# Kernel optimization log

Hardware: AMD Instinct MI355X
Metric: run time of the kernel (lower is better)

Reference implementation:

```python
import jax, jax.numpy as jnp
import numpy as np

N_NODES = 50000
N_EDGES = 800000
F_IN = 128      # n_alleles
HID = 64        # ge_hidden_dim
HEADS = 2       # gat_heads
LAT = 128       # latent_dim
N_PHEN = 50


def setup_inputs() -> dict:
    key = jax.random.key(0)
    ks = jax.random.split(key, 16)
    s = 0.05
    return {
        'x': jax.random.normal(ks[0], (N_NODES, F_IN), jnp.float32),
        'edge_index': jax.random.randint(ks[1], (2, N_EDGES), 0, N_NODES, jnp.int64),
        'pheno_idx': jnp.arange(N_PHEN, dtype=jnp.int64),
        'pheno_embedding': jax.random.normal(ks[2], (N_PHEN, F_IN), jnp.float32) * 0.1,
        'Wl1': jax.random.normal(ks[3], (F_IN, HEADS * HID), jnp.float32) * s,
        'Wr1': jax.random.normal(ks[4], (F_IN, HEADS * HID), jnp.float32) * s,
        'att1': jax.random.normal(ks[5], (HEADS, HID), jnp.float32) * s,
        'b1': jax.random.normal(ks[6], (HEADS * HID,), jnp.float32) * s,
        'Wl2': jax.random.normal(ks[7], (HEADS * HID, LAT), jnp.float32) * s,
        'Wr2': jax.random.normal(ks[8], (HEADS * HID, LAT), jnp.float32) * s,
        'att2': jax.random.normal(ks[9], (1, LAT), jnp.float32) * s,
        'b2': jax.random.normal(ks[10], (LAT,), jnp.float32) * s,
        'Wp': jax.random.normal(ks[11], (LAT, LAT), jnp.float32) * s,
        'bp': jax.random.normal(ks[12], (LAT,), jnp.float32) * s,
    }


def gatv2_conv(x, src, dst, Wl, Wr, att, bias, concat):
    # PyG GATv2Conv: e = att . leaky_relu(Wl x_src + Wr x_dst, 0.2), softmax over dst
    N = x.shape[0]
    H, C = att.shape
    xl = (x @ Wl).reshape(N, H, C)
    xr = (x @ Wr).reshape(N, H, C)
    feat = jax.nn.leaky_relu(xl[src] + xr[dst], 0.2)         # [E,H,C]
    logits = jnp.einsum('ehc,hc->eh', feat, att)             # [E,H]
    m = jax.ops.segment_max(logits, dst, num_segments=N)     # [N,H]
    ex = jnp.exp(logits - m[dst])
    denom = jax.ops.segment_sum(ex, dst, num_segments=N)
    alpha = ex / denom[dst]                                  # [E,H]
    out = jax.ops.segment_sum(alpha[:, :, None] * xl[src], dst, num_segments=N)
    out = out.reshape(N, H * C) if concat else out.mean(axis=1)
    return out + bias


def reference(x, edge_index, pheno_idx, pheno_embedding,
              Wl1, Wr1, att1, b1, Wl2, Wr2, att2, b2, Wp, bp):
    N = x.shape[0]
    # learnable phenotype node embeddings replace their input features
    x = x.at[pheno_idx].set(pheno_embedding)
    # PyG default: add self loops
    loops = jnp.arange(N, dtype=edge_index.dtype)
    src = jnp.concatenate([edge_index[0], loops])
    dst = jnp.concatenate([edge_index[1], loops])
    h = jax.nn.leaky_relu(gatv2_conv(x, src, dst, Wl1, Wr1, att1, b1, True), 0.01)
    h = gatv2_conv(h, src, dst, Wl2, Wr2, att2, b2, False)
    graph_embedding = h[pheno_idx].mean(axis=0, keepdims=True)  # [1, LAT]
    return graph_embedding @ Wp + bp
```

## Files before the change

### kernel.cpp

```cpp
#include <hip/hip_runtime.h>
#include <hip/hip_fp16.h>
#include <cstdint>

#define F_DIM 128

typedef _Float16 f16x8 __attribute__((ext_vector_type(8)));
typedef float f32x4 __attribute__((ext_vector_type(4)));

__device__ __forceinline__ float lrelu(float x, float s) { return x > 0.f ? x : s * x; }

template<int W>
__device__ __forceinline__ float redg(float p) {
  #pragma unroll
  for (int d = 1; d < W; d <<= 1) p += __shfl_xor(p, d);
  return p;
}

__device__ __forceinline__ int cidx(const int* __restrict__ csr, int k, int last) {
  return csr[k <= last ? k : last];
}

__device__ __forceinline__ __half2 shfl_xor_h2(__half2 v, int m) {
  union { __half2 h; int i; } u; u.h = v;
  u.i = __shfl_xor(u.i, m);
  return u.h;
}

typedef _Float16 h2v __attribute__((ext_vector_type(2)));
__device__ __forceinline__ __half2 h2max(__half2 a, __half2 b) {
  union { __half2 h; h2v v; } ua, ub, ur;
  ua.h = a; ub.h = b;
  ur.v = __builtin_elementwise_max(ua.v, ub.v);
  return ur.h;
}

__global__ void k_init(int* __restrict__ deg, int* __restrict__ rowmap, int N) {
  int i = blockIdx.x * blockDim.x + threadIdx.x;
  if (i < N) { deg[i] = 0; rowmap[i] = -1; }
}

__global__ void k_hist_rowmap(const int* __restrict__ dst, int* __restrict__ deg,
                              const int* __restrict__ pidx, int* __restrict__ rowmap,
                              int E, int P) {
  int e = blockIdx.x * blockDim.x + threadIdx.x;
  if (e < E) atomicAdd(&deg[dst[e]], 1);
  if (e < P) rowmap[pidx[e]] = e;
}

__global__ void k_scan_reduce(const int* __restrict__ deg, int* __restrict__ bsum, int N) {
  __shared__ int ts[256];
  int tid = threadIdx.x;
  int base = blockIdx.x * 1024 + tid * 4;
  int s = 0;
  #pragma unroll
  for (int j = 0; j < 4; ++j) { int idx = base + j; if (idx < N) s += deg[idx]; }
  ts[tid] = s; __syncthreads();
  for (int d = 128; d > 0; d >>= 1) { if (tid < d) ts[tid] += ts[tid + d]; __syncthreads(); }
  if (tid == 0) bsum[blockIdx.x] = ts[0];
}

__global__ void k_scan_single(int* __restrict__ bsum, int nb) {
  int l = threadIdx.x;
  int v = (l < nb) ? bsum[l] : 0;
  int orig = v;
  #pragma unroll
  for (int d = 1; d < 64; d <<= 1) { int t = __shfl_up(v, d); if (l >= d) v += t; }
  if (l < nb) bsum[l] = v - orig;
}

__global__ void k_scan_final(const int* __restrict__ deg, const int* __restrict__ bsum,
                             int* __restrict__ rowStart, int* __restrict__ cursor,
                             int N, int E) {
  __shared__ int ts[256];
  int tid = threadIdx.x;
  int base = blockIdx.x * 1024 + tid * 4;
  int v[4]; int s = 0;
  #pragma unroll
  for (int j = 0; j < 4; ++j) { int idx = base + j; v[j] = (idx < N) ? deg[idx] : 0; s += v[j]; }
  ts[tid] = s; __syncthreads();
  for (int d = 1; d < 256; d <<= 1) {
    int t = (tid >= d) ? ts[tid - d] : 0;
    __syncthreads();
    ts[tid] += t;
    __syncthreads();
  }
  int off = bsum[blockIdx.x] + ts[tid] - s;
  #pragma unroll
  for (int j = 0; j < 4; ++j) {
    int idx = base + j;
    if (idx < N) { rowStart[idx] = off; cursor[idx] = off; }
    off += v[j];
  }
  if (blockIdx.x == 0 && tid == 0) rowStart[N] = E;
}

__global__ void k_scatter_edges(const int* __restrict__ src, const int* __restrict__ dst,
                                int* __restrict__ cur, int* __restrict__ csr, int E) {
  int e = blockIdx.x * blockDim.x + threadIdx.x;
  if (e >= E) return;
  int d = dst[e];
  int p = atomicAdd(&cur[d], 1);
  csr[p] = src[e];
}

__global__ void k_cvt_x(const float* __restrict__ x, const float* __restrict__ pe,
                        const int* __restrict__ rowmap, __half* __restrict__ xh, int N) {
  int t = blockIdx.x * 256 + threadIdx.x;
  if (t >= N * 16) return;
  int row = t >> 4, seg = (t & 15) * 8;
  const float* src = &x[(size_t)row * 128 + seg];
  int rm = rowmap[row];
  if (rm >= 0) src = &pe[(size_t)rm * 128 + seg];
  float4 v0 = *reinterpret_cast<const float4*>(src);
  float4 v1 = *reinterpret_cast<const float4*>(src + 4);
  union { __half h[8]; float4 f; } pk;
  pk.h[0] = __float2half(v0.x); pk.h[1] = __float2half(v0.y);
  pk.h[2] = __float2half(v0.z); pk.h[3] = __float2half(v0.w);
  pk.h[4] = __float2half(v1.x); pk.h[5] = __float2half(v1.y);
  pk.h[6] = __float2half(v1.z); pk.h[7] = __float2half(v1.w);
  *reinterpret_cast<float4*>(&xh[(size_t)row * 128 + seg]) = pk.f;
}

__global__ void k_cvt_w(const float* __restrict__ Wl1, const float* __restrict__ Wr1,
                        const float* __restrict__ Wl2, const float* __restrict__ Wr2,
                        __half* __restrict__ Wt1, __half* __restrict__ Wt2) {
  int t = blockIdx.x * 256 + threadIdx.x;
  if (t >= 2 * 32768) return;
  int layer = t >> 15;
  int i = t & 32767;
  int c = i >> 7, k = i & 127;
  const float* Wl = layer ? Wl2 : Wl1;
  const float* Wr = layer ? Wr2 : Wr1;
  float v = (c < 128) ? Wl[k * 128 + c] : Wr[k * 128 + (c - 128)];
  (layer ? Wt2 : Wt1)[i] = __float2half(v);
}

__global__ __launch_bounds__(256) void k_gemm_mfma(
    const __half* __restrict__ Ah, const __half* __restrict__ Wt,
    __half* __restrict__ outL, __half* __restrict__ outR, int M)
{
  int cg = blockIdx.x & 3;
  int rg = blockIdx.x >> 2;
  int wv = threadIdx.x >> 6;
  int l  = threadIdx.x & 63;
  int rowb = rg * 128 + wv * 32;
  int colb = cg * 64;
  int lr = l & 15;
  int lq = l >> 4;
  f32x4 acc[2][4] = {};
  #pragma unroll
  for (int ks = 0; ks < 4; ++ks) {
    int k0 = ks * 32 + lq * 8;
    int r0 = rowb + lr;      if (r0 > M - 1) r0 = M - 1;
    int r1 = rowb + 16 + lr; if (r1 > M - 1) r1 = M - 1;
    f16x8 a0 = *reinterpret_cast<const f16x8*>(&Ah[(size_t)r0 * 128 + k0]);
    f16x8 a1 = *reinterpret_cast<const f16x8*>(&Ah[(size_t)r1 * 128 + k0]);
    f16x8 b[4];
    #pragma unroll
    for (int c = 0; c < 4; ++c)
      b[c] = *reinterpret_cast<const f16x8*>(&Wt[(size_t)(colb + c * 16 + lr) * 128 + k0]);
    #pragma unroll
    for (int c = 0; c < 4; ++c) {
      acc[0][c] = __builtin_amdgcn_mfma_f32_16x16x32_f16(a0, b[c], acc[0][c], 0, 0, 0);
      acc[1][c] = __builtin_amdgcn_mfma_f32_16x16x32_f16(a1, b[c], acc[1][c], 0, 0, 0);
    }
  }
  #pragma unroll
  for (int r = 0; r < 2; ++r) {
    #pragma unroll
    for (int j = 0; j < 4; ++j) {
      int grow = rowb + r * 16 + lq * 4 + j;
      if (grow < M) {
        #pragma unroll
        for (int c = 0; c < 4; ++c) {
          int gcol = colb + c * 16 + lr;
          __half v = __float2half(acc[r][c][j]);
          if (gcol < 128) outL[(size_t)grow * 128 + gcol] = v;
          else            outR[(size_t)grow * 128 + (gcol - 128)] = v;
        }
      }
    }
  }
}

template<int RW, bool OUTER_LRELU, bool HOUT>
__global__ __launch_bounds__(64) void k_agg(
    const __half* __restrict__ xl, const __half* __restrict__ xr,
    const float* __restrict__ att, const float* __restrict__ bias,
    const int* __restrict__ rowStart, const int* __restrict__ csr,
    float* __restrict__ outf, __half* __restrict__ outh, int N)
{
  int n = blockIdx.x;
  int l = threadIdx.x;
  int slot = l >> 4;
  int q = l & 15;
  int ch = q * 8;
  size_t nb = (size_t)n * F_DIM + ch;

  float4 rawr = *reinterpret_cast<const float4*>(&xr[nb]);
  float4 rawl = *reinterpret_cast<const float4*>(&xl[nb]);
  const __half2* xrn = reinterpret_cast<const __half2*>(&rawr);
  const __half2* xln = reinterpret_cast<const __half2*>(&rawl);
  __half2 av[4];
  #pragma unroll
  for (int i = 0; i < 4; ++i)
    av[i] = __float22half2_rn(*reinterpret_cast<const float2*>(&att[ch + 2 * i]));
  const __half2 slope = __float2half2_rn(0.2f);

  float denom;
  __half2 acc[4];
  {
    __half2 pr = __float2half2_rn(0.f);
    #pragma unroll
    for (int i = 0; i < 4; ++i) {
      __half2 t = __hadd2(xln[i], xrn[i]);
      __half2 lr = h2max(t, __hmul2(t, slope));
      pr = __hfma2(lr, av[i], pr);
    }
    float2 pf = __half22float2(pr);
    float p = redg<RW>(pf.x + pf.y);
    float w = (slot == 0) ? __expf(p) : 0.f;
    denom = w;
    __half2 wh = __float2half2_rn(w);
    #pragma unroll
    for (int i = 0; i < 4; ++i) acc[i] = __hmul2(xln[i], wh);
  }

  int e0 = rowStart[n], e1 = rowStart[n + 1];
  int last = e1 - 1;
  if (e0 < e1) {
    auto ld = [&](int k) {
      int s = cidx(csr, k, last);
      return *reinterpret_cast<const float4*>(&xl[(size_t)s * F_DIM + ch]);
    };
    auto proc = [&](float4 rawv, int ebase) {
      const __half2* xv = reinterpret_cast<const __half2*>(&rawv);
      __half2 pr = __float2half2_rn(0.f);
      #pragma unroll
      for (int i = 0; i < 4; ++i) {
        __half2 t = __hadd2(xv[i], xrn[i]);
        __half2 lr = h2max(t, __hmul2(t, slope));
        pr = __hfma2(lr, av[i], pr);
      }
      float2 pf = __half22float2(pr);
      float p = redg<RW>(pf.x + pf.y);
      float wE = ((ebase + slot) <= last) ? __expf(p) : 0.f;
      denom += wE;
      __half2 wh = __float2half2_rn(wE);
      #pragma unroll
      for (int i = 0; i < 4; ++i) acc[i] = __hfma2(xv[i], wh, acc[i]);
    };
    float4 v0 = ld(e0 + slot);
    float4 v1 = ld(e0 + 4 + slot);
    for (int e = e0; e < e1; e += 4) {
      bool m2 = (e + 8) < e1;
      float4 v2;
      if (m2) v2 = ld(e + 8 + slot);
      proc(v0, e);
      v0 = v1;
      if (m2) v1 = v2;
    }
  }

  denom += __shfl_xor(denom, 16);
  denom += __shfl_xor(denom, 32);
  #pragma unroll
  for (int i = 0; i < 4; ++i) {
    acc[i] = __hadd2(acc[i], shfl_xor_h2(acc[i], 16));
    acc[i] = __hadd2(acc[i], shfl_xor_h2(acc[i], 32));
  }

  if (slot == 0) {
    float inv = 1.0f / denom;
    float o[8];
    #pragma unroll
    for (int i = 0; i < 4; ++i) {
      float2 a2 = __half22float2(acc[i]);
      o[2 * i + 0] = fmaf(a2.x, inv, bias[ch + 2 * i + 0]);
      o[2 * i + 1] = fmaf(a2.y, inv, bias[ch + 2 * i + 1]);
    }
    if (OUTER_LRELU) {
      #pragma unroll
      for (int i = 0; i < 8; ++i) o[i] = lrelu(o[i], 0.01f);
    }
    if (HOUT) {
      union { __half h[8]; float4 f; } pk;
      #pragma unroll
      for (int i = 0; i < 8; ++i) pk.h[i] = __float2half(o[i]);
      *reinterpret_cast<float4*>(&outh[nb]) = pk.f;
    } else {
      *reinterpret_cast<float4*>(&outf[nb]) = *reinterpret_cast<float4*>(&o[0]);
      *reinterpret_cast<float4*>(&outf[nb + 4]) = *reinterpret_cast<float4*>(&o[4]);
    }
  }
}

__global__ void k_final(const float* __restrict__ h2, const int* __restrict__ pidx,
                        const float* __restrict__ Wp, const float* __restrict__ bp,
                        float* __restrict__ out, int P)
{
  __shared__ float ge[F_DIM];
  int t = threadIdx.x;
  float s0 = 0.f, s1 = 0.f;
  for (int i = 0; i + 1 < P; i += 2) {
    s0 += h2[(size_t)pidx[i] * F_DIM + t];
    s1 += h2[(size_t)pidx[i + 1] * F_DIM + t];
  }
  if (P & 1) s0 += h2[(size_t)pidx[P - 1] * F_DIM + t];
  ge[t] = (s0 + s1) / (float)P;
  __syncthreads();
  float a0 = 0.f, a1 = 0.f, a2 = 0.f, a3 = 0.f;
  for (int k = 0; k < F_DIM; k += 4) {
    a0 = fmaf(ge[k + 0], Wp[(k + 0) * F_DIM + t], a0);
    a1 = fmaf(ge[k + 1], Wp[(k + 1) * F_DIM + t], a1);
    a2 = fmaf(ge[k + 2], Wp[(k + 2) * F_DIM + t], a2);
    a3 = fmaf(ge[k + 3], Wp[(k + 3) * F_DIM + t], a3);
  }
  out[t] = bp[t] + ((a0 + a1) + (a2 + a3));
}

extern "C" void kernel_launch(void* const* d_in, const int* in_sizes, int n_in,
                              void* d_out, int out_size, void* d_ws, size_t ws_size,
                              hipStream_t stream)
{
  const float* x    = (const float*)d_in[0];
  const int*   ei   = (const int*)d_in[1];
  const int*   pidx = (const int*)d_in[2];
  const float* pe   = (const float*)d_in[3];
  const float* Wl1  = (const float*)d_in[4];
  const float* Wr1  = (const float*)d_in[5];
  const float* att1 = (const float*)d_in[6];
  const float* b1   = (const float*)d_in[7];
  const float* Wl2  = (const float*)d_in[8];
  const float* Wr2  = (const float*)d_in[9];
  const float* att2 = (const float*)d_in[10];
  const float* b2   = (const float*)d_in[11];
  const float* Wp   = (const float*)d_in[12];
  const float* bp   = (const float*)d_in[13];
  float* outp = (float*)d_out;

  const int N = in_sizes[0] / F_DIM;
  const int E = in_sizes[1] / 2;
  const int P = in_sizes[2];
  const int* esrc = ei;
  const int* edst = ei + E;

  char* w = (char*)d_ws;
  size_t off = 0;
  auto alloc = [&](size_t bytes) -> void* {
    void* p = w + off;
    off += (bytes + 255) & ~(size_t)255;
    return p;
  };
  const size_t NF = (size_t)N * F_DIM * sizeof(float);
  float*  A   = (float*)alloc(NF);
  __half* Bh  = (__half*)alloc(NF / 2);
  __half* Ch  = (__half*)alloc(NF / 2);
  __half* Xh  = (__half*)alloc(NF / 2);
  __half* H1h = (__half*)alloc(NF / 2);
  __half* Wt1 = (__half*)alloc(2 * 32768 * sizeof(__half));
  __half* Wt2 = Wt1 + 32768;
  int* rowStart = (int*)alloc((size_t)(N + 1) * sizeof(int));
  int* cursor   = (int*)alloc((size_t)N * sizeof(int));
  int* deg      = (int*)alloc((size_t)N * sizeof(int));
  int* bsum     = (int*)alloc(64 * sizeof(int));
  int* rowmap   = (int*)alloc((size_t)N * sizeof(int));
  int* csr      = (int*)alloc((size_t)E * sizeof(int));

  const int nb = (N + 1023) / 1024;
  const int RG = (N + 127) / 128;

  k_init<<<(N + 255) / 256, 256, 0, stream>>>(deg, rowmap, N);
  k_hist_rowmap<<<(E + 255) / 256, 256, 0, stream>>>(edst, deg, pidx, rowmap, E, P);
  k_scan_reduce<<<nb, 256, 0, stream>>>(deg, bsum, N);
  k_scan_single<<<1, 64, 0, stream>>>(bsum, nb);
  k_scan_final<<<nb, 256, 0, stream>>>(deg, bsum, rowStart, cursor, N, E);
  k_scatter_edges<<<(E + 255) / 256, 256, 0, stream>>>(esrc, edst, cursor, csr, E);

  k_cvt_x<<<(N * 16 + 255) / 256, 256, 0, stream>>>(x, pe, rowmap, Xh, N);
  k_cvt_w<<<256, 256, 0, stream>>>(Wl1, Wr1, Wl2, Wr2, Wt1, Wt2);

  k_gemm_mfma<<<RG * 4, 256, 0, stream>>>(Xh, Wt1, Bh, Ch, N);
  k_agg<8, true, true><<<N, 64, 0, stream>>>(Bh, Ch, att1, b1, rowStart, csr,
                                             nullptr, H1h, N);
  k_gemm_mfma<<<RG * 4, 256, 0, stream>>>(H1h, Wt2, Bh, Ch, N);
  k_agg<16, false, false><<<N, 64, 0, stream>>>(Bh, Ch, att2, b2, rowStart, csr,
                                                A, nullptr, N);
  k_final<<<1, 128, 0, stream>>>(A, pidx, Wp, bp, outp, P);
}
```

Baseline: 327.0 us.

## Partition edge histogram/scatter by XCD slot and fuse init/convert kernels

The histogram and edge-scatter kernels now assign blocks to eight destination-range slots (blockIdx mod 8), so that atomics on a given destination range come from blocks that likely run on the same XCD, which is meant to keep atomic traffic local to one L2. Every slot's blocks re-read the whole dst array, which multiplies index reads by eight. The init kernel is fused with the weight conversion, and the edge scatter is fused with the x conversion as separate block ranges, which cuts kernel launches and lets independent work overlap.

```diff
diff --git a/kernel.cpp b/kernel.cpp
--- a/kernel.cpp
+++ b/kernel.cpp
@@ -3,6 +3,7 @@
 #include <cstdint>
 
 #define F_DIM 128
+#define NSLOT 8
 
 typedef _Float16 f16x8 __attribute__((ext_vector_type(8)));
 typedef float f32x4 __attribute__((ext_vector_type(4)));
@@ -34,17 +35,41 @@
   return ur.h;
 }
 
-__global__ void k_init(int* __restrict__ deg, int* __restrict__ rowmap, int N) {
-  int i = blockIdx.x * blockDim.x + threadIdx.x;
-  if (i < N) { deg[i] = 0; rowmap[i] = -1; }
-}
-
-__global__ void k_hist_rowmap(const int* __restrict__ dst, int* __restrict__ deg,
-                              const int* __restrict__ pidx, int* __restrict__ rowmap,
-                              int E, int P) {
-  int e = blockIdx.x * blockDim.x + threadIdx.x;
-  if (e < E) atomicAdd(&deg[dst[e]], 1);
-  if (e < P) rowmap[pidx[e]] = e;
+__global__ void k_init_cvtw(int* __restrict__ deg, int* __restrict__ rowmap, int N, int NB1,
+                            const float* __restrict__ Wl1, const float* __restrict__ Wr1,
+                            const float* __restrict__ Wl2, const float* __restrict__ Wr2,
+                            __half* __restrict__ Wt1, __half* __restrict__ Wt2) {
+  int bid = blockIdx.x;
+  if (bid < NB1) {
+    int i = bid * 256 + threadIdx.x;
+    if (i < N) { deg[i] = 0; rowmap[i] = -1; }
+  } else {
+    int t = (bid - NB1) * 256 + threadIdx.x;
+    if (t < 2 * 32768) {
+      int layer = t >> 15;
+      int i = t & 32767;
+      int c = i >> 7, k = i & 127;
+      const float* Wl = layer ? Wl2 : Wl1;
+      const float* Wr = layer ? Wr2 : Wr1;
+      float v = (c < 128) ? Wl[k * 128 + c] : Wr[k * 128 + (c - 128)];
+      (layer ? Wt2 : Wt1)[i] = __float2half(v);
+    }
+  }
+}
+
+__global__ void k_hist_xcd(const int* __restrict__ dst, int* __restrict__ deg,
+                           const int* __restrict__ pidx, int* __restrict__ rowmap,
+                           int E, int P, int C, int span) {
+  if (blockIdx.x == 0) {
+    for (int i = threadIdx.x; i < P; i += 256) rowmap[pidx[i]] = i;
+  }
+  int s = blockIdx.x & (NSLOT - 1);
+  int cb = blockIdx.x >> 3;
+  int lo = s * span, hi = lo + span;
+  for (int e = cb * 256 + threadIdx.x; e < E; e += C * 256) {
+    int d = dst[e];
+    if (d >= lo && d < hi) atomicAdd(&deg[d], 1);
+  }
 }
 
 __global__ void k_scan_reduce(const int* __restrict__ deg, int* __restrict__ bsum, int N) {
@@ -94,45 +119,41 @@
   if (blockIdx.x == 0 && tid == 0) rowStart[N] = E;
 }
 
-__global__ void k_scatter_edges(const int* __restrict__ src, const int* __restrict__ dst,
-                                int* __restrict__ cur, int* __restrict__ csr, int E) {
-  int e = blockIdx.x * blockDim.x + threadIdx.x;
-  if (e >= E) return;
-  int d = dst[e];
-  int p = atomicAdd(&cur[d], 1);
-  csr[p] = src[e];
-}
-
-__global__ void k_cvt_x(const float* __restrict__ x, const float* __restrict__ pe,
-                        const int* __restrict__ rowmap, __half* __restrict__ xh, int N) {
-  int t = blockIdx.x * 256 + threadIdx.x;
-  if (t >= N * 16) return;
-  int row = t >> 4, seg = (t & 15) * 8;
-  const float* src = &x[(size_t)row * 128 + seg];
-  int rm = rowmap[row];
-  if (rm >= 0) src = &pe[(size_t)rm * 128 + seg];
-  float4 v0 = *reinterpret_cast<const float4*>(src);
-  float4 v1 = *reinterpret_cast<const float4*>(src + 4);
-  union { __half h[8]; float4 f; } pk;
-  pk.h[0] = __float2half(v0.x); pk.h[1] = __float2half(v0.y);
-  pk.h[2] = __float2half(v0.z); pk.h[3] = __float2half(v0.w);
-  pk.h[4] = __float2half(v1.x); pk.h[5] = __float2half(v1.y);
-  pk.h[6] = __float2half(v1.z); pk.h[7] = __float2half(v1.w);
-  *reinterpret_cast<float4*>(&xh[(size_t)row * 128 + seg]) = pk.f;
-}
-
-__global__ void k_cvt_w(const float* __restrict__ Wl1, const float* __restrict__ Wr1,
-                        const float* __restrict__ Wl2, const float* __restrict__ Wr2,
-                        __half* __restrict__ Wt1, __half* __restrict__ Wt2) {
-  int t = blockIdx.x * 256 + threadIdx.x;
-  if (t >= 2 * 32768) return;
-  int layer = t >> 15;
-  int i = t & 32767;
-  int c = i >> 7, k = i & 127;
-  const float* Wl = layer ? Wl2 : Wl1;
-  const float* Wr = layer ? Wr2 : Wr1;
-  float v = (c < 128) ? Wl[k * 128 + c] : Wr[k * 128 + (c - 128)];
-  (layer ? Wt2 : Wt1)[i] = __float2half(v);
+__global__ void k_scatter_xcd_cvtx(const int* __restrict__ src, const int* __restrict__ dst,
+                                   int* __restrict__ cur, int* __restrict__ csr,
+                                   int E, int C, int span, int N, int CVTB,
+                                   const float* __restrict__ x, const float* __restrict__ pe,
+                                   const int* __restrict__ rowmap, __half* __restrict__ xh) {
+  int bid = blockIdx.x;
+  int SC = NSLOT * C;
+  if (bid < SC) {
+    int s = bid & (NSLOT - 1);
+    int cb = bid >> 3;
+    int lo = s * span, hi = lo + span;
+    for (int e = cb * 256 + threadIdx.x; e < E; e += C * 256) {
+      int d = dst[e];
+      if (d >= lo && d < hi) {
+        int p = atomicAdd(&cur[d], 1);
+        csr[p] = src[e];
+      }
+    }
+  } else {
+    int nt = N * 16;
+    for (int t = (bid - SC) * 256 + threadIdx.x; t < nt; t += CVTB * 256) {
+      int row = t >> 4, seg = (t & 15) * 8;
+      const float* sp = &x[(size_t)row * 128 + seg];
+      int rm = rowmap[row];
+      if (rm >= 0) sp = &pe[(size_t)rm * 128 + seg];
+      float4 v0 = *reinterpret_cast<const float4*>(sp);
+      float4 v1 = *reinterpret_cast<const float4*>(sp + 4);
+      union { __half h[8]; float4 f; } pk;
+      pk.h[0] = __float2half(v0.x); pk.h[1] = __float2half(v0.y);
+      pk.h[2] = __float2half(v0.z); pk.h[3] = __float2half(v0.w);
+      pk.h[4] = __float2half(v1.x); pk.h[5] = __float2half(v1.y);
+      pk.h[6] = __float2half(v1.z); pk.h[7] = __float2half(v1.w);
+      *reinterpret_cast<float4*>(&xh[(size_t)row * 128 + seg]) = pk.f;
+    }
+  }
 }
 
 __global__ __launch_bounds__(256) void k_gemm_mfma(
@@ -367,18 +388,20 @@
   int* rowmap   = (int*)alloc((size_t)N * sizeof(int));
   int* csr      = (int*)alloc((size_t)E * sizeof(int));
 
-  const int nb = (N + 1023) / 1024;
-  const int RG = (N + 127) / 128;
-
-  k_init<<<(N + 255) / 256, 256, 0, stream>>>(deg, rowmap, N);
-  k_hist_rowmap<<<(E + 255) / 256, 256, 0, stream>>>(edst, deg, pidx, rowmap, E, P);
+  const int nb   = (N + 1023) / 1024;
+  const int RG   = (N + 127) / 128;
+  const int NB1  = (N + 255) / 256;
+  const int span = (N + NSLOT - 1) / NSLOT;
+  const int C    = 128;
+  const int CVTB = 1024;
+
+  k_init_cvtw<<<NB1 + 256, 256, 0, stream>>>(deg, rowmap, N, NB1, Wl1, Wr1, Wl2, Wr2, Wt1, Wt2);
+  k_hist_xcd<<<NSLOT * C, 256, 0, stream>>>(edst, deg, pidx, rowmap, E, P, C, span);
   k_scan_reduce<<<nb, 256, 0, stream>>>(deg, bsum, N);
   k_scan_single<<<1, 64, 0, stream>>>(bsum, nb);
   k_scan_final<<<nb, 256, 0, stream>>>(deg, bsum, rowStart, cursor, N, E);
-  k_scatter_edges<<<(E + 255) / 256, 256, 0, stream>>>(esrc, edst, cursor, csr, E);
-
-  k_cvt_x<<<(N * 16 + 255) / 256, 256, 0, stream>>>(x, pe, rowmap, Xh, N);
-  k_cvt_w<<<256, 256, 0, stream>>>(Wl1, Wr1, Wl2, Wr2, Wt1, Wt2);
+  k_scatter_xcd_cvtx<<<NSLOT * C + CVTB, 256, 0, stream>>>(
+      esrc, edst, cursor, csr, E, C, span, N, CVTB, x, pe, rowmap, Xh);
 
   k_gemm_mfma<<<RG * 4, 256, 0, stream>>>(Xh, Wt1, Bh, Ch, N);
   k_agg<8, true, true><<<N, 64, 0, stream>>>(Bh, Ch, att1, b1, rowStart, csr,
```

Measured after the change: 313.0 us. 4.3% less time.
